# Kernel tuning notes

Measured on AMD Instinct MI355X. Metric: run time of the kernel, lower is better.

## Reference

```python
import jax, jax.numpy as jnp
import numpy as np

B, D, T, STRIDE = 16, 512, 2048, 4
SIGMA_SQUARE = 5.0
L = -(-T // STRIDE)  # ceil(T/stride) = 512


def setup_inputs() -> dict:
    key = jax.random.key(0)
    k1, k2, k3 = jax.random.split(key, 3)
    x = jax.random.normal(k1, (B, D, T), dtype=jnp.float32)
    # score conv: Conv1d(hdim, 1, 1, bias=False) == a single weight vector over D
    # (zero-initialized in the module; use small random values for a meaningful test)
    w = jax.random.normal(k2, (D,), dtype=jnp.float32) * 0.01
    x_lengths = jax.random.randint(k3, (B,), T // 2, T + 1)
    x_mask = jnp.arange(T)[None, :] < x_lengths[:, None]  # [B, T] bool
    return {"x": x, "w": w, "x_mask": x_mask, "x_lengths": x_lengths}


def reference(x, w, x_mask, x_lengths):
    maskf = x_mask.astype(x.dtype)  # [B, T]
    z_lengths = jnp.ceil(x_lengths.astype(x.dtype) / STRIDE).astype(jnp.int32)  # [B]
    z_mask = x_mask[:, ::STRIDE]  # [B, L]

    # score = exp(conv1x1(x)) * mask ; cum-sum position score
    score = jnp.exp(jnp.einsum('bdt,d->bt', x, w)) * maskf  # [B, T]
    cum = jnp.cumsum(score, axis=-1)  # [B, T]
    norm = (cum - cum[:, :1]) / (cum[:, -1:] - cum[:, :1]) \
           * (z_lengths[:, None].astype(x.dtype) - 1.0)  # [B, T]

    # monotonic-rate regularizer (get_score_loss)
    diff = norm[:, 1:] - norm[:, :-1]  # [B, T-1]
    score_loss = ((jax.nn.relu(diff - 1.0) * maskf[:, 1:]).sum(axis=-1)
                  / (x_lengths.astype(x.dtype) - 1.0)).mean()

    # masked Gaussian distance -> softmax over T -> alignment-weighted sum
    idx = jnp.arange(L, dtype=x.dtype)  # [L]
    dist = -SIGMA_SQUARE * (idx[None, None, :] - norm[:, :, None]) ** 2  # [B, T, L]
    dist = jnp.swapaxes(dist, 1, 2)  # [B, L, T]
    dist = jnp.where(x_mask[:, None, :], dist, -jnp.inf)
    alignment = jax.nn.softmax(dist, axis=-1) * z_mask[:, :, None].astype(x.dtype)  # [B, L, T]

    z = jnp.einsum('blt,bdt->bdl', alignment, x)  # [B, D, L]
    return z, z_mask, z_lengths, alignment, score_loss
```

## Files before the change

kernel.cpp:

```cpp
#include <hip/hip_runtime.h>
#include <cstddef>

#define Bn 16
#define Dn 512
#define Tn 2048
#define Ln 512
#define NLT 64

__global__ __launch_bounds__(256) void scorefill_kernel(const float* __restrict__ x,
                                                        const float* __restrict__ w,
                                                        const int* __restrict__ xlen,
                                                        float* __restrict__ score,
                                                        float4* __restrict__ align4) {
    int bid = blockIdx.x;
    int tid = threadIdx.x;

    if (bid >= 512) {
        const size_t NT = (size_t)Bn * Ln * Tn / 16;
        size_t i = (size_t)(bid - 512) * 256 + tid;
        float4 z4 = make_float4(0.f, 0.f, 0.f, 0.f);
        align4[i]          = z4;
        align4[i + NT]     = z4;
        align4[i + 2 * NT] = z4;
        align4[i + 3 * NT] = z4;
        return;
    }

    int b   = bid >> 5;
    int tc  = bid & 31;
    int xl  = xlen[b];
    int t0c = tc * 64;
    if (t0c >= xl) {
        if (tid < 16)
            *(float4*)&score[b * Tn + t0c + tid * 4] = make_float4(0.f, 0.f, 0.f, 0.f);
        return;
    }
    int tq  = tid & 15;
    int dg  = tid >> 4;
    int t0  = t0c + tq * 4;
    const float* xb = x + (size_t)b * Dn * Tn + t0;
    float4 acc = make_float4(0.f, 0.f, 0.f, 0.f);
    int dbase = dg * 32;
#pragma unroll 8
    for (int i = 0; i < 32; ++i) {
        int d = dbase + i;
        float4 v = *(const float4*)&xb[(size_t)d * Tn];
        float wd = w[d];
        acc.x = fmaf(v.x, wd, acc.x);
        acc.y = fmaf(v.y, wd, acc.y);
        acc.z = fmaf(v.z, wd, acc.z);
        acc.w = fmaf(v.w, wd, acc.w);
    }
    __shared__ float4 red[16][16];
    red[dg][tq] = acc;
    __syncthreads();
    if (tid < 16) {
        float4 s = red[0][tid];
#pragma unroll
        for (int g = 1; g < 16; ++g) {
            float4 r = red[g][tid];
            s.x += r.x; s.y += r.y; s.z += r.z; s.w += r.w;
        }
        int t = t0c + tid * 4;
        float4 o;
        o.x = (t + 0 < xl) ? __expf(s.x) : 0.f;
        o.y = (t + 1 < xl) ? __expf(s.y) : 0.f;
        o.z = (t + 2 < xl) ? __expf(s.z) : 0.f;
        o.w = (t + 3 < xl) ? __expf(s.w) : 0.f;
        *(float4*)&score[b * Tn + t] = o;
    }
}

__global__ __launch_bounds__(256) void scan_kernel(const float* __restrict__ score,
                                                   const int* __restrict__ xlen,
                                                   float* __restrict__ norm,
                                                   float* __restrict__ loss_part,
                                                   float* __restrict__ zmask_out,
                                                   float* __restrict__ zlen_out,
                                                   int* __restrict__ wlo,
                                                   int* __restrict__ whi,
                                                   float* __restrict__ sMout,
                                                   float* __restrict__ sIout) {
    int b = blockIdx.x, tid = threadIdx.x;
    int xl = xlen[b];
    int zl = (xl + 3) >> 2;
    const float* sc = score + b * Tn;

    __shared__ float sNorm[Tn];
    __shared__ int   sTC[Ln];

    float v[8]; float s = 0.f;
#pragma unroll
    for (int k = 0; k < 8; ++k) { v[k] = sc[tid * 8 + k]; s += v[k]; }

    float ps = s;
#pragma unroll
    for (int off = 1; off < 64; off <<= 1) {
        float n = __shfl_up(ps, off, 64);
        if ((tid & 63) >= off) ps += n;
    }
    __shared__ float wsum[4];
    if ((tid & 63) == 63) wsum[tid >> 6] = ps;
    __syncthreads();
    float base = 0.f;
#pragma unroll
    for (int wv = 0; wv < 4; ++wv) if (wv < (tid >> 6)) base += wsum[wv];
    float total = wsum[0] + wsum[1] + wsum[2] + wsum[3];
    float cum0  = sc[0];
    float scale = (float)(zl - 1) / (total - cum0);

    float run = base + ps - s;
    float nv[8];
#pragma unroll
    for (int k = 0; k < 8; ++k) {
        run += v[k];
        float xx = (run - cum0) * scale;
        nv[k] = xx;
        norm[b * Tn + tid * 8 + k] = xx;
        sNorm[tid * 8 + k] = xx;
    }

    float ls = 0.f;
#pragma unroll
    for (int k = 0; k < 8; ++k) {
        int t = tid * 8 + k;
        if (t >= 1 && t < xl) {
            float diff = v[k] * scale;
            ls += fmaxf(diff - 1.0f, 0.f);
        }
    }
#pragma unroll
    for (int off = 32; off; off >>= 1) ls += __shfl_down(ls, off, 64);
    __shared__ float lw[4];
    if ((tid & 63) == 0) lw[tid >> 6] = ls;

    for (int l = tid; l < Ln; l += 256)
        zmask_out[b * Ln + l] = (l * 4 < xl) ? 1.f : 0.f;
    if (tid == 0) zlen_out[b] = (float)zl;

    for (int i = tid; i < NLT; i += 256) {
        wlo[b * NLT + i] = xl;
        whi[b * NLT + i] = xl;
    }
    for (int l = tid; l < Ln; l += 256) sTC[l] = xl - 1;
    __syncthreads();
    if (tid == 0) loss_part[b] = (lw[0] + lw[1] + lw[2] + lw[3]) / (float)(xl - 1);

#pragma unroll
    for (int k = 0; k < 8; ++k) {
        int t = tid * 8 + k;
        float vv = nv[k];
        float p  = (t == 0) ? -1e9f : sNorm[t - 1];
        int lsr = (int)floorf((p + 1.5f) * 0.125f) + 1; if (lsr < 0) lsr = 0;
        int ler = (int)floorf((vv + 1.5f) * 0.125f);    if (ler > NLT - 1) ler = NLT - 1;
        for (int lt = lsr; lt <= ler; ++lt) wlo[b * NLT + lt] = t;
        int hs = (int)ceilf((p - 8.5f) * 0.125f);       if (hs < 0) hs = 0;
        int he = (int)ceilf((vv - 8.5f) * 0.125f) - 1;  if (he > NLT - 1) he = NLT - 1;
        for (int lt = hs; lt <= he; ++lt) whi[b * NLT + lt] = t;
        int cs = (int)floorf(p) + 1;  if (cs < 0) cs = 0;
        int ce = (int)floorf(vv);     if (ce > Ln - 1) ce = Ln - 1;
        for (int l = cs; l <= ce; ++l) sTC[l] = t;
    }
    __syncthreads();

    for (int l = tid; l < Ln; l += 256) {
        float mv = 0.f, iv = 0.f;
        if (l < zl) {
            int tc2 = sTC[l];
            float d1 = (float)l - sNorm[tc2];
            float m  = -5.f * d1 * d1;
            if (tc2 > 0) { float d0v = (float)l - sNorm[tc2 - 1]; float c = -5.f * d0v * d0v; m = fmaxf(m, c); }
            int lo = (l >= 2) ? sTC[l - 2] : 0;
            int hi = (l + 2 <= zl - 1) ? sTC[l + 2] : xl;
            int tcm1 = (tc2 > 0) ? tc2 - 1 : 0;
            if (lo > tcm1) lo = tcm1;
            int tcp1 = (tc2 + 1 < xl) ? tc2 + 1 : xl;
            if (hi < tcp1) hi = tcp1;
            float ssum = 0.f;
            for (int t = lo; t < hi; ++t) {
                float df = (float)l - sNorm[t];
                ssum += __expf(-5.f * df * df - m);
            }
            mv = m; iv = 1.f / ssum;
        }
        sMout[b * Ln + l] = mv;
        sIout[b * Ln + l] = iv;
    }
}

__global__ __launch_bounds__(256) void z_kernel(const float* __restrict__ x,
                                                const float* __restrict__ norm,
                                                const int* __restrict__ xlen,
                                                const int* __restrict__ wlo,
                                                const int* __restrict__ whi,
                                                const float* __restrict__ sM,
                                                const float* __restrict__ sI,
                                                const float* __restrict__ loss_part,
                                                float* __restrict__ align,
                                                float* __restrict__ z,
                                                float* __restrict__ out_loss) {
    int tid = threadIdx.x;
    int bid = blockIdx.x;
    if (bid == 0 && tid == 0) {
        float s = 0.f;
        for (int i = 0; i < Bn; ++i) s += loss_part[i];
        out_loss[0] = s / (float)Bn;
    }
    int swz = (bid & 7) * 256 + (bid >> 3);
    int b   = swz >> 7;
    int rem = swz & 127;
    int lt  = rem >> 1;
    int dh  = rem & 1;
    int l0  = lt * 8;
    int xl  = xlen[b];
    int zl  = (xl + 3) >> 2;
    int d   = dh * 256 + tid;
    size_t zr = (size_t)(b * Dn + d) * Ln + l0;

    if (l0 >= zl) {
        float4 z4 = make_float4(0.f, 0.f, 0.f, 0.f);
        *(float4*)&z[zr] = z4; *(float4*)&z[zr + 4] = z4;
        return;
    }

    int tlo = wlo[b * NLT + lt];
    int thi = whi[b * NLT + lt];
    if (thi > xl) thi = xl;
    int tA = tlo & ~15;

    __shared__ float sA[64][8];
    const float* nb = norm + b * Tn;
    const float* xr = x + (size_t)(b * Dn + d) * Tn;

    int al = tid >> 5;
    int as = tid & 31;
    float ml = sM[b * Ln + l0 + al];
    float il = sI[b * Ln + l0 + al];
    float lr = (float)(l0 + al);
    float* ar = align + (size_t)(b * Ln + l0 + al) * Tn;

    float acc[8] = {};
    float4 rx[16];

    for (int t0 = tA; t0 < thi; t0 += 64) {
#pragma unroll
        for (int j = 0; j < 16; ++j) {
            int tj = t0 + 4 * j;
            if (tj > Tn - 4) tj = Tn - 4;
            rx[j] = *(const float4*)&xr[tj];
        }
        {
            int t1 = t0 + as, t2 = t1 + 32;
            float a1 = 0.f, a2 = 0.f;
            if (t1 < thi) { float df = lr - nb[t1]; a1 = __expf(fmaf(-5.f * df, df, -ml)) * il; }
            if (t2 < thi) { float df = lr - nb[t2]; a2 = __expf(fmaf(-5.f * df, df, -ml)) * il; }
            sA[as][al] = a1;
            sA[as + 32][al] = a2;
            if (dh == 0) {
                if (t1 < thi) ar[t1] = a1;
                if (t2 < thi) ar[t2] = a2;
            }
        }
        __syncthreads();
#pragma unroll
        for (int c = 0; c < 16; ++c) {
            float4 xv = rx[c];
#pragma unroll
            for (int e = 0; e < 4; ++e) {
                int s = 4 * c + e;
                float xs = ((const float*)&xv)[e];
                float4 a0 = *(const float4*)&sA[s][0];
                float4 a1 = *(const float4*)&sA[s][4];
                acc[0] = fmaf(xs, a0.x, acc[0]);
                acc[1] = fmaf(xs, a0.y, acc[1]);
                acc[2] = fmaf(xs, a0.z, acc[2]);
                acc[3] = fmaf(xs, a0.w, acc[3]);
                acc[4] = fmaf(xs, a1.x, acc[4]);
                acc[5] = fmaf(xs, a1.y, acc[5]);
                acc[6] = fmaf(xs, a1.z, acc[6]);
                acc[7] = fmaf(xs, a1.w, acc[7]);
            }
        }
        __syncthreads();
    }

    *(float4*)&z[zr]     = make_float4(acc[0], acc[1], acc[2], acc[3]);
    *(float4*)&z[zr + 4] = make_float4(acc[4], acc[5], acc[6], acc[7]);
}

extern "C" void kernel_launch(void* const* d_in, const int* in_sizes, int n_in,
                              void* d_out, int out_size, void* d_ws, size_t ws_size,
                              hipStream_t stream) {
    const float* x    = (const float*)d_in[0];
    const float* w    = (const float*)d_in[1];
    const int*   xlen = (const int*)d_in[3];
    float* out = (float*)d_out;

    const size_t OFF_Z     = 0;
    const size_t OFF_ZMASK = (size_t)Bn * Dn * Ln;
    const size_t OFF_ZLEN  = OFF_ZMASK + (size_t)Bn * Ln;
    const size_t OFF_ALIGN = OFF_ZLEN + Bn;
    const size_t OFF_LOSS  = OFF_ALIGN + (size_t)Bn * Ln * Tn;

    float* score     = (float*)d_ws;
    float* norm      = score + (size_t)Bn * Tn;
    float* loss_part = norm + (size_t)Bn * Tn;
    int*   wlo       = (int*)(loss_part + Bn);
    int*   whi       = wlo + Bn * NLT;
    float* sMw       = (float*)(whi + Bn * NLT);
    float* sIw       = sMw + (size_t)Bn * Ln;

    scorefill_kernel<<<512 + 4096, 256, 0, stream>>>(x, w, xlen, score,
                                                     (float4*)(out + OFF_ALIGN));
    scan_kernel<<<Bn, 256, 0, stream>>>(score, xlen, norm, loss_part,
                                        out + OFF_ZMASK, out + OFF_ZLEN,
                                        wlo, whi, sMw, sIw);
    z_kernel<<<Bn * NLT * 2, 256, 0, stream>>>(x, norm, xlen, wlo, whi,
                                               sMw, sIw, loss_part,
                                               out + OFF_ALIGN, out + OFF_Z,
                                               out + OFF_LOSS);
}
```

Baseline: 55.28 us.

## Fuse scan into score kernel using per-batch release/acquire flags

Merges the scan kernel into the score/fill kernel as 16 extra blocks that spin on per-chunk flags published with release stores by the score blocks. This removes a kernel launch boundary so the per-batch scan can start as soon as its batch's scores are ready, overlapping with the alignment zero-fill. The scan blocks reset the flags afterwards so later calls work. It relies on the scan blocks being scheduled after or alongside the score blocks to avoid deadlock, and spinning blocks occupy CU slots while they wait.

```diff
diff --git a/kernel.cpp b/kernel.cpp
--- a/kernel.cpp
+++ b/kernel.cpp
@@ -6,16 +6,77 @@
 #define Tn 2048
 #define Ln 512
 #define NLT 64
+#define MAGIC 0x5EED5EEDu
 
 __global__ __launch_bounds__(256) void scorefill_kernel(const float* __restrict__ x,
                                                         const float* __restrict__ w,
                                                         const int* __restrict__ xlen,
                                                         float* __restrict__ score,
-                                                        float4* __restrict__ align4) {
+                                                        float4* __restrict__ align4,
+                                                        unsigned* __restrict__ flags,
+                                                        float* __restrict__ norm,
+                                                        float* __restrict__ loss_part,
+                                                        float* __restrict__ zmask_out,
+                                                        float* __restrict__ zlen_out,
+                                                        int* __restrict__ wlo,
+                                                        int* __restrict__ whi,
+                                                        float* __restrict__ sMout,
+                                                        float* __restrict__ sIout) {
     int bid = blockIdx.x;
     int tid = threadIdx.x;
 
-    if (bid >= 512) {
+    if (bid < 512) {
+        int b   = bid >> 5;
+        int tc  = bid & 31;
+        int xl  = xlen[b];
+        int t0c = tc * 64;
+        if (t0c < xl) {
+            int tq  = tid & 15;
+            int dg  = tid >> 4;
+            int t0  = t0c + tq * 4;
+            const float* xb = x + (size_t)b * Dn * Tn + t0;
+            float4 acc = make_float4(0.f, 0.f, 0.f, 0.f);
+            int dbase = dg * 32;
+#pragma unroll 8
+            for (int i = 0; i < 32; ++i) {
+                int d = dbase + i;
+                float4 v = *(const float4*)&xb[(size_t)d * Tn];
+                float wd = w[d];
+                acc.x = fmaf(v.x, wd, acc.x);
+                acc.y = fmaf(v.y, wd, acc.y);
+                acc.z = fmaf(v.z, wd, acc.z);
+                acc.w = fmaf(v.w, wd, acc.w);
+            }
+            __shared__ float4 red[16][16];
+            red[dg][tq] = acc;
+            __syncthreads();
+            if (tid < 16) {
+                float4 s = red[0][tid];
+#pragma unroll
+                for (int g = 1; g < 16; ++g) {
+                    float4 r = red[g][tid];
+                    s.x += r.x; s.y += r.y; s.z += r.z; s.w += r.w;
+                }
+                int t = t0c + tid * 4;
+                float4 o;
+                o.x = (t + 0 < xl) ? __expf(s.x) : 0.f;
+                o.y = (t + 1 < xl) ? __expf(s.y) : 0.f;
+                o.z = (t + 2 < xl) ? __expf(s.z) : 0.f;
+                o.w = (t + 3 < xl) ? __expf(s.w) : 0.f;
+                *(float4*)&score[b * Tn + t] = o;
+            }
+        } else {
+            if (tid < 16)
+                *(float4*)&score[b * Tn + t0c + tid * 4] = make_float4(0.f, 0.f, 0.f, 0.f);
+        }
+        __syncthreads();
+        if (tid == 0)
+            __hip_atomic_store(&flags[bid], MAGIC, __ATOMIC_RELEASE,
+                               __HIP_MEMORY_SCOPE_AGENT);
+        return;
+    }
+
+    if (bid < 512 + 4096) {
         const size_t NT = (size_t)Bn * Ln * Tn / 16;
         size_t i = (size_t)(bid - 512) * 256 + tid;
         float4 z4 = make_float4(0.f, 0.f, 0.f, 0.f);
@@ -26,62 +87,13 @@
         return;
     }
 
-    int b   = bid >> 5;
-    int tc  = bid & 31;
-    int xl  = xlen[b];
-    int t0c = tc * 64;
-    if (t0c >= xl) {
-        if (tid < 16)
-            *(float4*)&score[b * Tn + t0c + tid * 4] = make_float4(0.f, 0.f, 0.f, 0.f);
-        return;
-    }
-    int tq  = tid & 15;
-    int dg  = tid >> 4;
-    int t0  = t0c + tq * 4;
-    const float* xb = x + (size_t)b * Dn * Tn + t0;
-    float4 acc = make_float4(0.f, 0.f, 0.f, 0.f);
-    int dbase = dg * 32;
-#pragma unroll 8
-    for (int i = 0; i < 32; ++i) {
-        int d = dbase + i;
-        float4 v = *(const float4*)&xb[(size_t)d * Tn];
-        float wd = w[d];
-        acc.x = fmaf(v.x, wd, acc.x);
-        acc.y = fmaf(v.y, wd, acc.y);
-        acc.z = fmaf(v.z, wd, acc.z);
-        acc.w = fmaf(v.w, wd, acc.w);
-    }
-    __shared__ float4 red[16][16];
-    red[dg][tq] = acc;
+    int b = bid - (512 + 4096);
+    if (tid < 32) {
+        while (__hip_atomic_load(&flags[b * 32 + tid], __ATOMIC_ACQUIRE,
+                                 __HIP_MEMORY_SCOPE_AGENT) != MAGIC) {}
+    }
     __syncthreads();
-    if (tid < 16) {
-        float4 s = red[0][tid];
-#pragma unroll
-        for (int g = 1; g < 16; ++g) {
-            float4 r = red[g][tid];
-            s.x += r.x; s.y += r.y; s.z += r.z; s.w += r.w;
-        }
-        int t = t0c + tid * 4;
-        float4 o;
-        o.x = (t + 0 < xl) ? __expf(s.x) : 0.f;
-        o.y = (t + 1 < xl) ? __expf(s.y) : 0.f;
-        o.z = (t + 2 < xl) ? __expf(s.z) : 0.f;
-        o.w = (t + 3 < xl) ? __expf(s.w) : 0.f;
-        *(float4*)&score[b * Tn + t] = o;
-    }
-}
-
-__global__ __launch_bounds__(256) void scan_kernel(const float* __restrict__ score,
-                                                   const int* __restrict__ xlen,
-                                                   float* __restrict__ norm,
-                                                   float* __restrict__ loss_part,
-                                                   float* __restrict__ zmask_out,
-                                                   float* __restrict__ zlen_out,
-                                                   int* __restrict__ wlo,
-                                                   int* __restrict__ whi,
-                                                   float* __restrict__ sMout,
-                                                   float* __restrict__ sIout) {
-    int b = blockIdx.x, tid = threadIdx.x;
+
     int xl = xlen[b];
     int zl = (xl + 3) >> 2;
     const float* sc = score + b * Tn;
@@ -186,6 +198,10 @@
         sMout[b * Ln + l] = mv;
         sIout[b * Ln + l] = iv;
     }
+
+    if (tid < 32)
+        __hip_atomic_store(&flags[b * 32 + tid], 0u, __ATOMIC_RELAXED,
+                           __HIP_MEMORY_SCOPE_AGENT);
 }
 
 __global__ __launch_bounds__(256) void z_kernel(const float* __restrict__ x,
@@ -309,12 +325,12 @@
     int*   whi       = wlo + Bn * NLT;
     float* sMw       = (float*)(whi + Bn * NLT);
     float* sIw       = sMw + (size_t)Bn * Ln;
-
-    scorefill_kernel<<<512 + 4096, 256, 0, stream>>>(x, w, xlen, score,
-                                                     (float4*)(out + OFF_ALIGN));
-    scan_kernel<<<Bn, 256, 0, stream>>>(score, xlen, norm, loss_part,
-                                        out + OFF_ZMASK, out + OFF_ZLEN,
-                                        wlo, whi, sMw, sIw);
+    unsigned* flags  = (unsigned*)(sIw + (size_t)Bn * Ln);
+
+    scorefill_kernel<<<512 + 4096 + Bn, 256, 0, stream>>>(
+        x, w, xlen, score, (float4*)(out + OFF_ALIGN), flags,
+        norm, loss_part, out + OFF_ZMASK, out + OFF_ZLEN,
+        wlo, whi, sMw, sIw);
     z_kernel<<<Bn * NLT * 2, 256, 0, stream>>>(x, norm, xlen, wlo, whi,
                                                sMw, sIw, loss_part,
                                                out + OFF_ALIGN, out + OFF_Z,
```

Result: slower. 68.97 us (+24.8%).

## Split score blocks finer, use two-stage reduction and nontemporal zero-fill stores

Applied to the files above, without the earlier changes.

The score projection now uses 1024 blocks covering 32 time steps each, with 16 d-values per thread, which doubles block-level parallelism for the D-reduction. The shared-memory reduction becomes two stages, 64 then 8 threads, instead of a serial 16-way sum. The zero-fill of the large alignment buffer switches to nontemporal vector stores so the writes avoid polluting the cache. Fewer columns per block means each block's loads are narrower, which may reduce coalescing efficiency.

```diff
diff --git a/kernel.cpp b/kernel.cpp
--- a/kernel.cpp
+++ b/kernel.cpp
@@ -7,42 +7,45 @@
 #define Ln 512
 #define NLT 64
 
+typedef float nfloat4 __attribute__((ext_vector_type(4)));
+
 __global__ __launch_bounds__(256) void scorefill_kernel(const float* __restrict__ x,
                                                         const float* __restrict__ w,
                                                         const int* __restrict__ xlen,
                                                         float* __restrict__ score,
-                                                        float4* __restrict__ align4) {
+                                                        float* __restrict__ align) {
     int bid = blockIdx.x;
     int tid = threadIdx.x;
 
-    if (bid >= 512) {
-        const size_t NT = (size_t)Bn * Ln * Tn / 16;
-        size_t i = (size_t)(bid - 512) * 256 + tid;
-        float4 z4 = make_float4(0.f, 0.f, 0.f, 0.f);
-        align4[i]          = z4;
-        align4[i + NT]     = z4;
-        align4[i + 2 * NT] = z4;
-        align4[i + 3 * NT] = z4;
+    if (bid >= 1024) {
+        const size_t NT = (size_t)Bn * Ln * Tn / 4;
+        nfloat4* a4 = (nfloat4*)align;
+        size_t i = (size_t)(bid - 1024) * 256 + tid;
+        nfloat4 z4 = {0.f, 0.f, 0.f, 0.f};
+        __builtin_nontemporal_store(z4, &a4[i]);
+        __builtin_nontemporal_store(z4, &a4[i + NT / 4]);
+        __builtin_nontemporal_store(z4, &a4[i + 2 * (NT / 4)]);
+        __builtin_nontemporal_store(z4, &a4[i + 3 * (NT / 4)]);
         return;
     }
 
-    int b   = bid >> 5;
-    int tc  = bid & 31;
+    int b   = bid >> 6;
+    int tc  = bid & 63;
     int xl  = xlen[b];
-    int t0c = tc * 64;
+    int t0c = tc * 32;
     if (t0c >= xl) {
-        if (tid < 16)
+        if (tid < 8)
             *(float4*)&score[b * Tn + t0c + tid * 4] = make_float4(0.f, 0.f, 0.f, 0.f);
         return;
     }
-    int tq  = tid & 15;
-    int dg  = tid >> 4;
-    int t0  = t0c + tq * 4;
+    int tq = tid & 7;
+    int dg = tid >> 3;
+    int t0 = t0c + tq * 4;
     const float* xb = x + (size_t)b * Dn * Tn + t0;
     float4 acc = make_float4(0.f, 0.f, 0.f, 0.f);
-    int dbase = dg * 32;
-#pragma unroll 8
-    for (int i = 0; i < 32; ++i) {
+    int dbase = dg * 16;
+#pragma unroll
+    for (int i = 0; i < 16; ++i) {
         int d = dbase + i;
         float4 v = *(const float4*)&xb[(size_t)d * Tn];
         float wd = w[d];
@@ -51,14 +54,27 @@
         acc.z = fmaf(v.z, wd, acc.z);
         acc.w = fmaf(v.w, wd, acc.w);
     }
-    __shared__ float4 red[16][16];
+    __shared__ float4 red[32][8];
+    __shared__ float4 red2[8][8];
     red[dg][tq] = acc;
     __syncthreads();
-    if (tid < 16) {
-        float4 s = red[0][tid];
-#pragma unroll
-        for (int g = 1; g < 16; ++g) {
-            float4 r = red[g][tid];
+    if (tid < 64) {
+        int q = tid & 7, g = tid >> 3;
+        float4 s0 = red[g * 4 + 0][q], s1 = red[g * 4 + 1][q];
+        float4 s2 = red[g * 4 + 2][q], s3 = red[g * 4 + 3][q];
+        float4 s;
+        s.x = (s0.x + s1.x) + (s2.x + s3.x);
+        s.y = (s0.y + s1.y) + (s2.y + s3.y);
+        s.z = (s0.z + s1.z) + (s2.z + s3.z);
+        s.w = (s0.w + s1.w) + (s2.w + s3.w);
+        red2[g][q] = s;
+    }
+    __syncthreads();
+    if (tid < 8) {
+        float4 s = red2[0][tid];
+#pragma unroll
+        for (int g = 1; g < 8; ++g) {
+            float4 r = red2[g][tid];
             s.x += r.x; s.y += r.y; s.z += r.z; s.w += r.w;
         }
         int t = t0c + tid * 4;
@@ -310,8 +326,8 @@
     float* sMw       = (float*)(whi + Bn * NLT);
     float* sIw       = sMw + (size_t)Bn * Ln;
 
-    scorefill_kernel<<<512 + 4096, 256, 0, stream>>>(x, w, xlen, score,
-                                                     (float4*)(out + OFF_ALIGN));
+    scorefill_kernel<<<1024 + 4096, 256, 0, stream>>>(x, w, xlen, score,
+                                                      out + OFF_ALIGN);
     scan_kernel<<<Bn, 256, 0, stream>>>(score, xlen, norm, loss_part,
                                         out + OFF_ZMASK, out + OFF_ZLEN,
                                         wlo, whi, sMw, sIw);
```

New measurement: 56.23 us. Within noise of the previous version (+1.7%).

## Zero only alignment entries outside each row's active window

Applied to the files above, without the earlier changes.

Previously the fill kernel zeroed the whole alignment tensor and the z kernel then overwrote the active window. Now the fill kernel zeroes only rows past z_length, and the z kernel zeroes the parts of each active row outside its [tlo, thi) window, splitting that work between the two d-halves. This removes the redundant full write of the large alignment output, which costs a lot of memory bandwidth. In exchange the z kernel does extra scattered stores and more index logic, and any gap in coverage would leave stale values.

```diff
diff --git a/kernel.cpp b/kernel.cpp
--- a/kernel.cpp
+++ b/kernel.cpp
@@ -11,18 +11,23 @@
                                                         const float* __restrict__ w,
                                                         const int* __restrict__ xlen,
                                                         float* __restrict__ score,
-                                                        float4* __restrict__ align4) {
+                                                        float* __restrict__ align) {
     int bid = blockIdx.x;
     int tid = threadIdx.x;
 
     if (bid >= 512) {
-        const size_t NT = (size_t)Bn * Ln * Tn / 16;
-        size_t i = (size_t)(bid - 512) * 256 + tid;
+        int r0 = (bid - 512) * 2;
         float4 z4 = make_float4(0.f, 0.f, 0.f, 0.f);
-        align4[i]          = z4;
-        align4[i + NT]     = z4;
-        align4[i + 2 * NT] = z4;
-        align4[i + 3 * NT] = z4;
+#pragma unroll
+        for (int rr = 0; rr < 2; ++rr) {
+            int r = r0 + rr;
+            int b = r >> 9, l = r & 511;
+            int zl = (xlen[b] + 3) >> 2;
+            if (l < zl) continue;
+            float4* row4 = (float4*)(align + (size_t)r * Tn);
+            row4[tid]       = z4;
+            row4[tid + 256] = z4;
+        }
         return;
     }
 
@@ -228,6 +233,27 @@
     if (thi > xl) thi = xl;
     int tA = tlo & ~15;
 
+    {
+        int start4 = (thi + 3) & ~3;
+        if (start4 > Tn) start4 = Tn;
+        int rest   = Tn - start4 - tA;
+        if (rest < 0) rest = 0;
+        int mid4   = start4 + ((rest >> 3) << 2);
+        int row    = tid >> 5, lane32 = tid & 31;
+        float* arw = align + (size_t)(b * Ln + l0 + row) * Tn;
+        float4 z4f = make_float4(0.f, 0.f, 0.f, 0.f);
+        if (dh == 0) {
+            for (int q = lane32; q < (tA >> 2); q += 32)
+                ((float4*)arw)[q] = z4f;
+            if (thi + lane32 < start4) arw[thi + lane32] = 0.f;
+            for (int q = (start4 >> 2) + lane32; q < (mid4 >> 2); q += 32)
+                ((float4*)arw)[q] = z4f;
+        } else {
+            for (int q = (mid4 >> 2) + lane32; q < (Tn >> 2); q += 32)
+                ((float4*)arw)[q] = z4f;
+        }
+    }
+
     __shared__ float sA[64][8];
     const float* nb = norm + b * Tn;
     const float* xr = x + (size_t)(b * Dn + d) * Tn;
@@ -311,7 +337,7 @@
     float* sIw       = sMw + (size_t)Bn * Ln;
 
     scorefill_kernel<<<512 + 4096, 256, 0, stream>>>(x, w, xlen, score,
-                                                     (float4*)(out + OFF_ALIGN));
+                                                     out + OFF_ALIGN);
     scan_kernel<<<Bn, 256, 0, stream>>>(score, xlen, norm, loss_part,
                                         out + OFF_ZMASK, out + OFF_ZLEN,
                                         wlo, whi, sMw, sIw);
```

Result: faster. 53.20 us (-3.8%).
